# Optimization experiments

Hardware: AMD Instinct MI355X
Metric: run time of the kernel (lower is better)

The kernel has to match this reference:

```python
import jax, jax.numpy as jnp
import numpy as np

EPS_NORM = 1e-12  # torch F.normalize eps
EPS_BN = 1e-5     # torch BatchNorm default eps


def l2norm(v, axis=-1):
    n = jnp.sqrt(jnp.sum(v * v, axis=axis, keepdims=True))
    return v / jnp.maximum(n, EPS_NORM)


def setup_inputs() -> dict:
    key = jax.random.key(0)
    k1, k2 = jax.random.split(key, 2)
    N, C, D, M, K = 4, 8, 196, 128, 64
    x = jax.random.normal(k1, (N, C, D, M), dtype=jnp.float32)
    # centroids ~ U[0,1) as in torch.rand
    centroids = jax.random.uniform(k2, (K, M), dtype=jnp.float32)
    alpha = 1.0
    # _init_params: conv.weight = 2*alpha*centroids (1x1 conv), conv.bias = -alpha*||centroids||
    conv_w = 2.0 * alpha * centroids            # (K, M)
    conv_b = -alpha * jnp.linalg.norm(centroids, axis=1)  # (K,)
    gamma = jnp.ones((C,), dtype=jnp.float32)   # BatchNorm3d(8) affine init
    beta = jnp.zeros((C,), dtype=jnp.float32)
    return {"x": x, "conv_w": conv_w, "conv_b": conv_b,
            "centroids": centroids, "gamma": gamma, "beta": beta}


def reference(x, conv_w, conv_b, centroids, gamma, beta):
    # x: (N, C, D, M) with M = descriptor dim, C must equal 8 (BatchNorm3d(8))
    xn = l2norm(x, axis=-1)  # descriptor-wise L2 norm (normalize_input=True)
    # 1x1 conv over channel axis M -> K cluster logits: (N, K, C, D)
    logits = jnp.einsum('ncdm,km->nkcd', xn, conv_w) + conv_b[None, :, None, None]
    soft_assign = jax.nn.softmax(logits, axis=1)  # over clusters K
    # residual: (N, K, C, D, M)
    residual = xn[:, None, :, :, :] - centroids[None, :, None, None, :]
    residual = residual * soft_assign[..., None]
    # permute to (N, C, D, K, M), intra-normalize over descriptor dim
    vlad = jnp.transpose(residual, (0, 2, 3, 1, 4))
    vlad = l2norm(vlad, axis=-1)
    # BatchNorm3d(8), training mode: stats over (N, D, K, M) per channel C
    mean = jnp.mean(vlad, axis=(0, 2, 3, 4), keepdims=True)
    var = jnp.mean((vlad - mean) ** 2, axis=(0, 2, 3, 4), keepdims=True)
    vlad = (vlad - mean) / jnp.sqrt(var + EPS_BN)
    vlad = vlad * gamma[None, :, None, None, None] + beta[None, :, None, None, None]
    N, C, D, K, M = vlad.shape
    vlad = vlad.reshape(N, C, D, K * M)
    return l2norm(vlad, axis=-1)
```

## Files before the change

kernel.cpp:

```cpp
#include <hip/hip_runtime.h>

#define NB 4
#define CB 8
#define DB 196
#define MBd 128
#define KBc 64
#define ROWS (NB*CB*DB)
#define RROWS 16
#define GRID3 (ROWS/RROWS)
#define RPB 7
#define GRID (ROWS/RPB)
#define CNTF 6422528.0f

typedef float floatx4 __attribute__((ext_vector_type(4)));

__device__ __forceinline__ float dot4(floatx4 a, floatx4 b){
    return fmaf(a.x,b.x, fmaf(a.y,b.y, fmaf(a.z,b.z, a.w*b.w)));
}

__global__ __launch_bounds__(256) void k_stats(const float* __restrict__ x,
                                               const float* __restrict__ cent,
                                               float* __restrict__ rn_ws,
                                               float* __restrict__ xrn_ws,
                                               float* __restrict__ sv_ws)
{
    __shared__ floatx4 xs4[RROWS*32];
    __shared__ float p2[256], px[256];
    __shared__ float rxrn[RROWS], rsxn[RROWS];
    __shared__ float svbuf[RROWS*68];

    const int t    = threadIdx.x;
    const int rb   = blockIdx.x * RROWS;
    const int lane = t & 63;
    const int rs   = t >> 6;
    const floatx4* c4 = (const floatx4*)cent;
    const floatx4* xg = (const floatx4*)x;

    floatx4 creg[32];
#pragma unroll
    for (int m4 = 0; m4 < 32; ++m4) creg[m4] = c4[lane*32 + m4];

    xs4[t]       = xg[rb*32 + t];
    xs4[256 + t] = xg[rb*32 + 256 + t];
    __syncthreads();

    {
        const int r = t >> 4, seg = t & 15;
        const floatx4 a = xs4[r*32 + seg*2];
        const floatx4 b = xs4[r*32 + seg*2 + 1];
        p2[t] = dot4(a,a) + dot4(b,b);
        px[t] = ((a.x+a.y)+(a.z+a.w)) + ((b.x+b.y)+(b.z+b.w));
    }
    __syncthreads();
    if (t < RROWS) {
        float s2 = 0.f, sx = 0.f;
#pragma unroll
        for (int j = 0; j < 16; ++j) { s2 += p2[t*16+j]; sx += px[t*16+j]; }
        const float xrn = __builtin_amdgcn_rsqf(s2);
        rxrn[t] = xrn;
        rsxn[t] = sx * xrn;
        xrn_ws[rb + t] = xrn;
    }

    float ssck = 0.f, opck = 1.f;
#pragma unroll
    for (int m4 = 0; m4 < 32; ++m4) {
        const floatx4 cv = creg[m4];
        ssck += (cv.x+cv.y)+(cv.z+cv.w);
        opck  = fmaf(cv.x,cv.x, fmaf(cv.y,cv.y, fmaf(cv.z,cv.z, fmaf(cv.w,cv.w, opck))));
    }
    __syncthreads();

#pragma unroll
    for (int rr = 0; rr < 4; ++rr) {
        const int r = rs + rr*4;
        float d = 0.f;
#pragma unroll
        for (int m4 = 0; m4 < 32; ++m4) {
            const floatx4 xv = xs4[r*32 + m4];
            d = fmaf(xv.x,creg[m4].x, fmaf(xv.y,creg[m4].y,
                 fmaf(xv.z,creg[m4].z, fmaf(xv.w,creg[m4].w, d))));
        }
        const float xrn = rxrn[r];
        const float rn  = __builtin_amdgcn_rsqf(fmaf(-2.f*xrn, d, opck));
        rn_ws[(size_t)(rb + r)*KBc + lane] = rn;
        svbuf[r*68 + lane] = (rsxn[r] - ssck) * rn;
    }
    __syncthreads();
    if (t < RROWS) {
        float s = 0.f;
#pragma unroll
        for (int j = 0; j < KBc; ++j) s += svbuf[t*68 + j];
        sv_ws[rb + t] = s;
    }
}

__global__ __launch_bounds__(256) void k_ab(const float* __restrict__ sv_ws,
                                            const float* __restrict__ gamma,
                                            const float* __restrict__ beta,
                                            float* __restrict__ ab_ws)
{
    __shared__ float red[256];
    const int c = blockIdx.x, t = threadIdx.x;
    float s = 0.f;
    for (int i = t; i < NB*DB; i += 256) {
        const int n = i / DB, d = i % DB;
        s += sv_ws[n*(CB*DB) + c*DB + d];
    }
    red[t] = s; __syncthreads();
#pragma unroll
    for (int sd = 128; sd >= 1; sd >>= 1) {
        if (t < sd) red[t] += red[t+sd];
        __syncthreads();
    }
    if (t == 0) {
        const float mean = red[0] / CNTF;
        const float var  = 0.0078125f - mean*mean;
        const float istd = __builtin_amdgcn_rsqf(var + 1e-5f);
        const float aa = istd * gamma[c];
        ab_ws[2*c]   = aa;
        ab_ws[2*c+1] = beta[c] - mean * aa;
    }
}

__global__ __launch_bounds__(256) void k_out(const float* __restrict__ x,
                                             const float* __restrict__ cent,
                                             const float* __restrict__ rn_ws,
                                             const float* __restrict__ xrn_ws,
                                             const float* __restrict__ sv_ws,
                                             const float* __restrict__ ab_ws,
                                             float* __restrict__ out)
{
    const int t   = threadIdx.x;
    const int row = blockIdx.x;
    const int c   = (row / DB) % CB;
    const int l = t & 63, w = t >> 6, li2 = l & 31, hi = l >> 5;
    const floatx4* c4 = (const floatx4*)cent;
    const floatx4* xg = (const floatx4*)x;

    const floatx4 xa  = xg[row*32 + li2];
    const float   xrn = xrn_ws[row];
    const float   SVr = sv_ws[row];
    const float   aa  = ab_ws[2*c];
    const float   bb  = ab_ws[2*c+1];
    floatx4 cv[8];
    float   rnv[8];
#pragma unroll
    for (int it = 0; it < 8; ++it) {
        const int k = it*8 + w*2 + hi;
        cv[it]  = c4[k*32 + li2];
        rnv[it] = rn_ws[(size_t)row*KBc + k];
    }

    const float rni = __builtin_amdgcn_rsqf(
        fmaf(2.f*aa*bb, SVr, fmaf(64.f*aa, aa, 8192.f*bb*bb)));
    const float f1  = aa * rni;
    const float c2v = bb * rni;
    const floatx4 va = xa * xrn;

    floatx4* outr = (floatx4*)out + (size_t)row*2048;
#pragma unroll
    for (int it = 0; it < 8; ++it) {
        const int k = it*8 + w*2 + hi;
        const float cc = f1 * rnv[it];
        floatx4 o1;
        o1.x = fmaf(va.x - cv[it].x, cc, c2v);
        o1.y = fmaf(va.y - cv[it].y, cc, c2v);
        o1.z = fmaf(va.z - cv[it].z, cc, c2v);
        o1.w = fmaf(va.w - cv[it].w, cc, c2v);
        outr[k*32 + li2] = o1;
    }
}

__global__ __launch_bounds__(256) void k_stats_f(const float* __restrict__ x,
                                                 const float* __restrict__ cent,
                                                 float* __restrict__ sv_ws,
                                                 float* __restrict__ partial,
                                                 float* __restrict__ opc_ws)
{
    __shared__ float cs[KBc*MBd];
    __shared__ float sopc[KBc];
    __shared__ float ssc[KBc];
    __shared__ float sp1[256], sp2[256];
    __shared__ float svp[RPB*4];
    __shared__ float sv7[RPB];

    const int t  = threadIdx.x;
    const int rb = blockIdx.x * RPB;
    const floatx4* c4 = (const floatx4*)cent;
    floatx4* cs4 = (floatx4*)cs;
#pragma unroll
    for (int i = 0; i < 8; ++i) cs4[i*256 + t] = c4[i*256 + t];
    __syncthreads();
    {
        const int kk = t >> 2, q = t & 3;
        const floatx4* crow = &cs4[kk*32 + q*8];
        float ps = 0.f, pc = 0.f;
#pragma unroll
        for (int f = 0; f < 8; ++f) { floatx4 v = crow[f]; ps += (v.x+v.y)+(v.z+v.w); pc += dot4(v,v); }
        sp1[t] = ps; sp2[t] = pc;
    }
    __syncthreads();
    if (t < KBc) {
        ssc[t]  = (sp1[4*t]+sp1[4*t+1])+(sp1[4*t+2]+sp1[4*t+3]);
        sopc[t] = 1.0f + ((sp2[4*t]+sp2[4*t+1])+(sp2[4*t+2]+sp2[4*t+3]));
    }
    __syncthreads();
    if (blockIdx.x == 0 && t < KBc) opc_ws[t] = sopc[t];

    const int l = t & 63, w = t >> 6, g = (l >> 4), li = l & 15;
    const floatx4* xg = (const floatx4*)x;
    for (int ri = 0; ri < RPB; ++ri) {
        const int row = rb + ri;
        floatx4 xa = xg[row*32 + li];
        floatx4 xb = xg[row*32 + 16 + li];
        float s2 = dot4(xa,xa) + dot4(xb,xb);
        float sx = ((xa.x+xa.y)+(xa.z+xa.w)) + ((xb.x+xb.y)+(xb.z+xb.w));
#pragma unroll
        for (int o = 8; o >= 1; o >>= 1) { s2 += __shfl_xor(s2,o,64); sx += __shfl_xor(sx,o,64); }
        const float xrn = __builtin_amdgcn_rsqf(s2);
        const float Sx  = sx * xrn;
        float sva = 0.f;
#pragma unroll
        for (int it = 0; it < 4; ++it) {
            const int k = it*16 + w*4 + g;
            float d = dot4(xa, cs4[k*32+li]) + dot4(xb, cs4[k*32+16+li]);
#pragma unroll
            for (int o = 8; o >= 1; o >>= 1) d += __shfl_xor(d,o,64);
            const float dn = xrn * d;
            const float rn = __builtin_amdgcn_rsqf(fmaf(-2.f, dn, sopc[k]));
            sva = fmaf(Sx - ssc[k], rn, sva);
        }
#pragma unroll
        for (int o = 32; o >= 1; o >>= 1) sva += __shfl_xor(sva,o,64);
        if (l == 0) svp[ri*4 + w] = sva * 0.0625f;
    }
    __syncthreads();
    if (t < RPB) {
        float s = (svp[4*t]+svp[4*t+1])+(svp[4*t+2]+svp[4*t+3]);
        sv_ws[rb + t] = s;
        sv7[t] = s;
    }
    __syncthreads();
    if (t == 0) {
        float s = 0.f;
#pragma unroll
        for (int i = 0; i < RPB; ++i) s += sv7[i];
        partial[blockIdx.x] = s;
    }
}

__global__ __launch_bounds__(256) void k_out_f(const float* __restrict__ x,
                                               const float* __restrict__ cent,
                                               const float* __restrict__ sv_ws,
                                               const float* __restrict__ partial,
                                               const float* __restrict__ opc_ws,
                                               const float* __restrict__ gamma,
                                               const float* __restrict__ beta,
                                               float* __restrict__ out)
{
    __shared__ float cs[KBc*MBd];
    __shared__ float sopc[KBc];
    __shared__ float sab[2];
    const int t  = threadIdx.x;
    const int rb = blockIdx.x * RPB;
    const int c  = (blockIdx.x / 28) % CB;
    const floatx4* c4 = (const floatx4*)cent;
    floatx4* cs4 = (floatx4*)cs;
#pragma unroll
    for (int i = 0; i < 8; ++i) cs4[i*256 + t] = c4[i*256 + t];
    if (t >= 64 && t < 128) sopc[t-64] = opc_ws[t-64];
    if (t < 64) {
        float s1 = 0.f;
        if (t < 56) {
            const int j0 = t, j1 = t + 56;
            const int b0 = (j0/28)*224 + c*28 + (j0%28);
            const int b1 = (j1/28)*224 + c*28 + (j1%28);
            s1 = partial[b0] + partial[b1];
        }
#pragma unroll
        for (int o = 32; o >= 1; o >>= 1) s1 += __shfl_xor(s1,o,64);
        if (t == 0) {
            const float mean = s1 / CNTF;
            const float var  = 0.0078125f - mean*mean;
            const float istd = __builtin_amdgcn_rsqf(var + 1e-5f);
            const float aa = istd * gamma[c];
            const float bb = beta[c] - mean * aa;
            sab[0] = aa; sab[1] = bb;
        }
    }
    __syncthreads();
    const float aa = sab[0], bb = sab[1];

    const int l = t & 63, w = t >> 6, g = (l >> 4), li = l & 15;
    const floatx4* xg = (const floatx4*)x;
    for (int ri = 0; ri < RPB; ++ri) {
        const int row = rb + ri;
        floatx4 xa = xg[row*32 + li];
        floatx4 xb = xg[row*32 + 16 + li];
        float s2 = dot4(xa,xa) + dot4(xb,xb);
#pragma unroll
        for (int o = 8; o >= 1; o >>= 1) s2 += __shfl_xor(s2,o,64);
        const float xrn = __builtin_amdgcn_rsqf(s2);
        const floatx4 va = xa * xrn, vb = xb * xrn;
        const float SVr = sv_ws[row];
        const float q   = fmaf(64.f*aa, aa, fmaf(2.f*aa*bb, SVr, 8192.f*bb*bb));
        const float rni = __builtin_amdgcn_rsqf(q);
        const float f1  = aa * rni;
        const float c2  = bb * rni;
        floatx4* outr = (floatx4*)out + (size_t)row*2048;
#pragma unroll
        for (int it = 0; it < 4; ++it) {
            const int k = it*16 + w*4 + g;
            const floatx4 cca = cs4[k*32+li];
            const floatx4 ccb = cs4[k*32+16+li];
            float d = dot4(va,cca) + dot4(vb,ccb);
#pragma unroll
            for (int o = 8; o >= 1; o >>= 1) d += __shfl_xor(d,o,64);
            const float rn = __builtin_amdgcn_rsqf(fmaf(-2.f, d, sopc[k]));
            const float cc = f1 * rn;
            floatx4 o1, o2;
            o1.x = fmaf(va.x - cca.x, cc, c2); o1.y = fmaf(va.y - cca.y, cc, c2);
            o1.z = fmaf(va.z - cca.z, cc, c2); o1.w = fmaf(va.w - cca.w, cc, c2);
            o2.x = fmaf(vb.x - ccb.x, cc, c2); o2.y = fmaf(vb.y - ccb.y, cc, c2);
            o2.z = fmaf(vb.z - ccb.z, cc, c2); o2.w = fmaf(vb.w - ccb.w, cc, c2);
            outr[k*32 + li]      = o1;
            outr[k*32 + 16 + li] = o2;
        }
    }
}

extern "C" void kernel_launch(void* const* d_in, const int* in_sizes, int n_in,
                              void* d_out, int out_size, void* d_ws, size_t ws_size,
                              hipStream_t stream)
{
    const float* x     = (const float*)d_in[0];
    const float* cent  = (const float*)d_in[3];
    const float* gamma = (const float*)d_in[4];
    const float* beta  = (const float*)d_in[5];
    float* out = (float*)d_out;

    const size_t need = (size_t)(ROWS*KBc + 2*ROWS + 16) * sizeof(float);
    if (ws_size >= need) {
        float* rn_ws   = (float*)d_ws;
        float* xrn_ws  = rn_ws + (size_t)ROWS*KBc;
        float* sv_ws   = xrn_ws + ROWS;
        float* ab_ws   = sv_ws + ROWS;
        hipLaunchKernelGGL(k_stats, dim3(GRID3), dim3(256), 0, stream,
                           x, cent, rn_ws, xrn_ws, sv_ws);
        hipLaunchKernelGGL(k_ab,    dim3(CB),    dim3(256), 0, stream,
                           sv_ws, gamma, beta, ab_ws);
        hipLaunchKernelGGL(k_out,   dim3(ROWS),  dim3(256), 0, stream,
                           x, cent, rn_ws, xrn_ws, sv_ws, ab_ws, out);
    } else {
        float* sv_ws   = (float*)d_ws;
        float* partial = sv_ws + ROWS;
        float* opc_ws  = partial + GRID;
        hipLaunchKernelGGL(k_stats_f, dim3(GRID), dim3(256), 0, stream,
                           x, cent, sv_ws, partial, opc_ws);
        hipLaunchKernelGGL(k_out_f,   dim3(GRID), dim3(256), 0, stream,
                           x, cent, sv_ws, partial, opc_ws, gamma, beta, out);
    }
}
```

Measured before the change: 51.96 us.

## Retile output kernel into 28-row by 8-cluster panels with shared-memory reuse

The output kernel used one block per row, each loading the full centroid table. It now uses one block per panel of 8 clusters by 28 rows. Each thread keeps a single centroid vector in registers, the normalized x rows and per-row scale factors are staged in LDS, and each thread loops over 28 rows writing strided output. This is meant to cut redundant centroid and scalar loads and reduce the block count, at the cost of an LDS barrier and writes that jump between rows.

```diff
diff --git a/kernel.cpp b/kernel.cpp
--- a/kernel.cpp
+++ b/kernel.cpp
@@ -8,6 +8,9 @@
 #define ROWS (NB*CB*DB)
 #define RROWS 16
 #define GRID3 (ROWS/RROWS)
+#define PNL 8
+#define GROWS 28
+#define OG2 ((KBc/PNL)*(ROWS/GROWS))
 #define RPB 7
 #define GRID (ROWS/RPB)
 #define CNTF 6422528.0f
@@ -131,44 +134,48 @@
                                              const float* __restrict__ ab_ws,
                                              float* __restrict__ out)
 {
+    __shared__ floatx4 xsn[GROWS*32];
+    __shared__ float   ccl[GROWS*PNL];
+    __shared__ float   c2l[GROWS];
     const int t   = threadIdx.x;
-    const int row = blockIdx.x;
-    const int c   = (row / DB) % CB;
-    const int l = t & 63, w = t >> 6, li2 = l & 31, hi = l >> 5;
+    const int p   = blockIdx.x & 7;
+    const int grp = blockIdx.x >> 3;
+    const int rb  = grp * GROWS;
+    const int c   = (rb / DB) % CB;
+    const int k0  = p * PNL;
     const floatx4* c4 = (const floatx4*)cent;
     const floatx4* xg = (const floatx4*)x;
 
-    const floatx4 xa  = xg[row*32 + li2];
-    const float   xrn = xrn_ws[row];
-    const float   SVr = sv_ws[row];
-    const float   aa  = ab_ws[2*c];
-    const float   bb  = ab_ws[2*c+1];
-    floatx4 cv[8];
-    float   rnv[8];
-#pragma unroll
-    for (int it = 0; it < 8; ++it) {
-        const int k = it*8 + w*2 + hi;
-        cv[it]  = c4[k*32 + li2];
-        rnv[it] = rn_ws[(size_t)row*KBc + k];
-    }
-
-    const float rni = __builtin_amdgcn_rsqf(
-        fmaf(2.f*aa*bb, SVr, fmaf(64.f*aa, aa, 8192.f*bb*bb)));
-    const float f1  = aa * rni;
-    const float c2v = bb * rni;
-    const floatx4 va = xa * xrn;
-
-    floatx4* outr = (floatx4*)out + (size_t)row*2048;
-#pragma unroll
-    for (int it = 0; it < 8; ++it) {
-        const int k = it*8 + w*2 + hi;
-        const float cc = f1 * rnv[it];
-        floatx4 o1;
-        o1.x = fmaf(va.x - cv[it].x, cc, c2v);
-        o1.y = fmaf(va.y - cv[it].y, cc, c2v);
-        o1.z = fmaf(va.z - cv[it].z, cc, c2v);
-        o1.w = fmaf(va.w - cv[it].w, cc, c2v);
-        outr[k*32 + li2] = o1;
+    const floatx4 cv = c4[(k0 + (t >> 5))*32 + (t & 31)];
+
+    for (int i = t; i < GROWS*32; i += 256) {
+        const int r = i >> 5;
+        xsn[i] = xg[(size_t)(rb + r)*32 + (i & 31)] * xrn_ws[rb + r];
+    }
+    const float aa = ab_ws[2*c], bb = ab_ws[2*c+1];
+    if (t < GROWS*PNL) {
+        const int r = t >> 3, kk = t & 7;
+        const int row = rb + r;
+        const float rni = __builtin_amdgcn_rsqf(
+            fmaf(2.f*aa*bb, sv_ws[row], fmaf(64.f*aa, aa, 8192.f*bb*bb)));
+        ccl[t] = aa * rni * rn_ws[(size_t)row*KBc + k0 + kk];
+        if (kk == 0) c2l[r] = bb * rni;
+    }
+    __syncthreads();
+
+    const int kk = t >> 5, m = t & 31;
+    floatx4* outb = (floatx4*)out + (size_t)rb*2048 + (k0 + kk)*32 + m;
+#pragma unroll
+    for (int r = 0; r < GROWS; ++r) {
+        const floatx4 v  = xsn[r*32 + m];
+        const float   cc = ccl[r*PNL + kk];
+        const float   c2 = c2l[r];
+        floatx4 o;
+        o.x = fmaf(v.x - cv.x, cc, c2);
+        o.y = fmaf(v.y - cv.y, cc, c2);
+        o.z = fmaf(v.z - cv.z, cc, c2);
+        o.w = fmaf(v.w - cv.w, cc, c2);
+        outb[(size_t)r*2048] = o;
     }
 }
 
@@ -350,7 +357,7 @@
                            x, cent, rn_ws, xrn_ws, sv_ws);
         hipLaunchKernelGGL(k_ab,    dim3(CB),    dim3(256), 0, stream,
                            sv_ws, gamma, beta, ab_ws);
-        hipLaunchKernelGGL(k_out,   dim3(ROWS),  dim3(256), 0, stream,
+        hipLaunchKernelGGL(k_out,   dim3(OG2),   dim3(256), 0, stream,
                            x, cent, rn_ws, xrn_ws, sv_ws, ab_ws, out);
     } else {
         float* sv_ws   = (float*)d_ws;
```

Result: slower. 54.60 us (+5.1%).
